# Kernel tuning notes

Measured on AMD Instinct MI355X. Metric: run time of the kernel, lower is better.

## Reference

```python
import jax, jax.numpy as jnp
import numpy as np

N_NODES = 50000
N_EDGES = 400000
N_GRAPHS = 128
IN_CH = 768
COND = 768
HID = 128
HEADS = 4


def _gat_conv(x, src, dst, W, att_src, att_dst, bias):
    """PyG-style GATConv (concat=True, negative_slope=0.2). x:[N,Fin], W:[Fin,H*D]."""
    N = x.shape[0]
    H, D = att_src.shape
    h = (x @ W).reshape(N, H, D)                      # [N,H,D]
    a_src = jnp.sum(h * att_src, axis=-1)             # [N,H]
    a_dst = jnp.sum(h * att_dst, axis=-1)             # [N,H]
    alpha = jax.nn.leaky_relu(a_src[src] + a_dst[dst], 0.2)   # [E,H]
    m = jax.ops.segment_max(alpha, dst, num_segments=N)       # per-dst max (stable softmax)
    alpha = jnp.exp(alpha - m[dst])
    s = jax.ops.segment_sum(alpha, dst, num_segments=N)
    alpha = alpha / (s[dst] + 1e-16)                  # PyG softmax eps
    msg = h[src] * alpha[:, :, None]                  # [E,H,D]
    out = jax.ops.segment_sum(msg, dst, num_segments=N)       # [N,H,D]
    return out.reshape(N, H * D) + bias


def setup_inputs() -> dict:
    key = jax.random.key(0)
    ks = jax.random.split(key, 12)

    def glorot(k, shape):
        fan = shape[0] + shape[-1]
        return jax.random.normal(k, shape, jnp.float32) * jnp.sqrt(2.0 / fan)

    x = jax.random.normal(ks[0], (N_NODES, IN_CH), jnp.float32)
    substring_embed = jax.random.normal(ks[1], (N_GRAPHS, COND), jnp.float32)
    edge_index = jax.random.randint(ks[2], (2, N_EDGES), 0, N_NODES)
    batch = jnp.sort(jax.random.randint(ks[3], (N_NODES,), 0, N_GRAPHS))

    W1 = glorot(ks[4], (IN_CH + COND, HEADS * HID))
    att_src1 = glorot(ks[5], (HEADS, HID))
    att_dst1 = glorot(ks[6], (HEADS, HID))
    b1 = jnp.zeros((HEADS * HID,), jnp.float32)

    W2 = glorot(ks[7], (HEADS * HID, 1 * HID))
    att_src2 = glorot(ks[8], (1, HID))
    att_dst2 = glorot(ks[9], (1, HID))
    b2 = jnp.zeros((HID,), jnp.float32)

    out_W = glorot(ks[10], (HID, 1))
    out_b = jnp.zeros((1,), jnp.float32)

    return {"x": x, "substring_embed": substring_embed,
            "W1": W1, "att_src1": att_src1, "att_dst1": att_dst1, "b1": b1,
            "W2": W2, "att_src2": att_src2, "att_dst2": att_dst2, "b2": b2,
            "out_W": out_W, "out_b": out_b,
            "edge_index": edge_index, "batch": batch}


def reference(x, substring_embed, W1, att_src1, att_dst1, b1,
              W2, att_src2, att_dst2, b2, out_W, out_b,
              edge_index, batch):
    N = x.shape[0]
    loops = jnp.arange(N)                              # PyG add_self_loops=True
    src = jnp.concatenate([edge_index[0], loops])
    dst = jnp.concatenate([edge_index[1], loops])

    h = jnp.concatenate([x, substring_embed[batch]], axis=-1)   # [N, IN+COND]
    h = jax.nn.relu(_gat_conv(h, src, dst, W1, att_src1, att_dst1, b1))
    h = jax.nn.relu(_gat_conv(h, src, dst, W2, att_src2, att_dst2, b2))
    out = (h @ out_W + out_b)[:, 0]                    # squeeze(-1) -> [N]
    return out
```

## Files before the change

### kernel.cpp

```cpp
#include <hip/hip_runtime.h>
#include <hip/hip_bf16.h>
#include <cstdint>
#include <cstddef>

#define NN 50000
#define NE 400000
#define NG 128
#define INCH 768
#define CONDCH 768
#define HIDD 128
#define NHEAD 4
#define F1 (NHEAD * HIDD)
#define F2 HIDD
#define MPAD 50176
#define CAP 64

typedef unsigned short ushort_t;
typedef float f32x4 __attribute__((ext_vector_type(4)));
typedef __bf16 bf16x8 __attribute__((ext_vector_type(8)));

typedef const void __attribute__((address_space(1))) as1_void;
typedef void __attribute__((address_space(3))) as3_void;

__device__ __forceinline__ void gload_lds16(const void* g, void* l) {
    __builtin_amdgcn_global_load_lds((as1_void*)g, (as3_void*)l, 16, 0, 0);
}

__device__ __forceinline__ ushort_t f2bf(float f) {
    uint32_t u = __float_as_uint(f);
    uint32_t r = (u + 0x7fffu + ((u >> 16) & 1u)) >> 16;
    return (ushort_t)r;
}
__device__ __forceinline__ uint32_t pack2(float a, float b) {
    return (uint32_t)f2bf(a) | ((uint32_t)f2bf(b) << 16);
}
__device__ __forceinline__ float bf_lo(uint32_t u) { return __uint_as_float(u << 16); }
__device__ __forceinline__ float bf_hi(uint32_t u) { return __uint_as_float(u & 0xffff0000u); }

#define R1 (F1 * INCH)
#define R2 (R1 + F1 * CONDCH)
#define R3 (R2 + F2 * F1)
#define CND4 (NG * CONDCH / 4)
__global__ __launch_bounds__(256) void k_prep(
    const float* __restrict__ W1, const float* __restrict__ W2, const float* __restrict__ cond,
    ushort_t* __restrict__ W1aT, ushort_t* __restrict__ W1cT, ushort_t* __restrict__ W2T,
    ushort_t* __restrict__ condb, int* __restrict__ cursor, int* __restrict__ csr_src)
{
    int idx = blockIdx.x * blockDim.x + threadIdx.x;
    if (idx < NN) {
        cursor[idx] = 1;
        csr_src[(size_t)idx * CAP] = idx;
    }
    if (idx < CND4) {
        float4 v = *(const float4*)(cond + (size_t)idx * 4);
        ushort4 o;
        o.x = f2bf(v.x); o.y = f2bf(v.y); o.z = f2bf(v.z); o.w = f2bf(v.w);
        *(ushort4*)(condb + (size_t)idx * 4) = o;
    }
    if (idx >= R3) return;
    if (idx < R1) {
        int n = idx / INCH, k = idx % INCH;
        W1aT[idx] = f2bf(W1[(size_t)k * F1 + n]);
    } else if (idx < R2) {
        int j = idx - R1;
        int n = j / CONDCH, k = j % CONDCH;
        W1cT[j] = f2bf(W1[(size_t)(INCH + k) * F1 + n]);
    } else {
        int j = idx - R2;
        int n = j / F1, k = j % F1;
        W2T[j] = f2bf(W2[(size_t)k * F2 + n]);
    }
}

__global__ __launch_bounds__(256) void k_scat(const int* __restrict__ ei,
                                              int* __restrict__ cursor,
                                              int* __restrict__ csr_src) {
    int e = blockIdx.x * blockDim.x + threadIdx.x;
    if (e >= NE) return;
    int src = ei[e];
    int dst = ei[NE + e];
    int pos = atomicAdd(&cursor[dst], 1);
    csr_src[(size_t)dst * CAP + pos] = src;
}

__global__ __launch_bounds__(256) void k_cvt8(const float* __restrict__ in,
                                              ushort_t* __restrict__ out, long n8) {
    long i = (long)blockIdx.x * blockDim.x + threadIdx.x;
    if (i >= n8) return;
    float4 v0 = *(const float4*)(in + i * 8);
    float4 v1 = *(const float4*)(in + i * 8 + 4);
    uint4 o;
    o.x = pack2(v0.x, v0.y);
    o.y = pack2(v0.z, v0.w);
    o.z = pack2(v1.x, v1.y);
    o.w = pack2(v1.z, v1.w);
    *(uint4*)(out + i * 8) = o;
}

template <int TM, bool ADD_GATHER, bool OUT_BF16, bool FUSE_ATT>
__global__ __launch_bounds__(TM * 2) void k_mgemm(
    const ushort_t* __restrict__ A, const ushort_t* __restrict__ BT, void* __restrict__ Cv,
    int M, int N, int K, int nBN,
    const float* __restrict__ G, const int* __restrict__ gidx,
    const float* __restrict__ attS, const float* __restrict__ attD,
    float* __restrict__ aS, float* __restrict__ aD, int attStride)
{
    constexpr int SA = TM * 64;
    constexpr int SB = 8192;
    __shared__ __align__(16) char smem[2 * SA + 2 * SB];
    char* sA = smem;
    char* sB = smem + 2 * SA;

    const int nwg = gridDim.x;
    const int orig = blockIdx.x;
    const int q = nwg >> 3, r = nwg & 7;
    const int xcd = orig & 7, sid = orig >> 3;
    const int wg = (xcd < r ? xcd * (q + 1) : r * (q + 1) + (xcd - r) * q) + sid;
    const int bx = wg / nBN, by = wg % nBN;

    const int tid = threadIdx.x;
    const int lane = tid & 63;
    const int wave = tid >> 6;
    const int wr = wave >> 1, wc = wave & 1;
    const int m0 = bx * TM, n0 = by * 128;

    const int sr = tid >> 2;
    const int sc = (tid & 3) * 8;
    const ushort_t* gA = A + (size_t)(m0 + sr) * K + sc;
    const ushort_t* gB = BT + (size_t)(n0 + sr) * K + sc;
    const int ldsw = wave * 1024;

    const int a_off = (wr * 64 + (lane & 15)) * 64 + (lane >> 4) * 16;
    const int b_off = (wc * 64 + (lane & 15)) * 64 + (lane >> 4) * 16;

    auto STAGE = [&](int kt, int b) {
        char* dA = sA + b * SA + ldsw;
        gload_lds16(gA + kt, dA);
        gload_lds16(gA + (size_t)(TM / 2) * K + kt, dA + SA / 2);
        char* dB = sB + b * SB + ldsw;
        gload_lds16(gB + kt, dB);
        if (TM == 128)
            gload_lds16(gB + (size_t)64 * K + kt, dB + 4096);
    };

    f32x4 acc[4][4];
#pragma unroll
    for (int i = 0; i < 4; i++)
#pragma unroll
        for (int j = 0; j < 4; j++) acc[i][j] = 0.f;

    STAGE(0, 0);
    const int nt = K / 32;
    for (int t = 0; t < nt; t++) {
        const int cur = t & 1;
        asm volatile("s_waitcnt vmcnt(0)" ::: "memory");
        __builtin_amdgcn_s_barrier();
        __builtin_amdgcn_sched_barrier(0);
        if (t + 1 < nt) STAGE((t + 1) * 32, cur ^ 1);
        bf16x8 af[4], bfr[4];
#pragma unroll
        for (int i = 0; i < 4; i++) af[i]  = *(const bf16x8*)(sA + cur * SA + a_off + i * 1024);
#pragma unroll
        for (int j = 0; j < 4; j++) bfr[j] = *(const bf16x8*)(sB + cur * SB + b_off + j * 1024);
#pragma unroll
        for (int i = 0; i < 4; i++)
#pragma unroll
            for (int j = 0; j < 4; j++)
                acc[i][j] = __builtin_amdgcn_mfma_f32_16x16x32_bf16(af[i], bfr[j], acc[i][j], 0, 0, 0);
    }

    float asv[4], adv[4];
    if (FUSE_ATT) {
#pragma unroll
        for (int j = 0; j < 4; j++) {
            int col = wc * 64 + j * 16 + (lane & 15);
            asv[j] = attS[by * 128 + col];
            adv[j] = attD[by * 128 + col];
        }
    }
    float* redS = (float*)smem;
    float* redD = (float*)smem + 2 * TM;

#pragma unroll
    for (int i = 0; i < 4; i++) {
        int mbase = m0 + wr * 64 + i * 16 + (lane >> 4) * 4;
#pragma unroll
        for (int rr = 0; rr < 4; rr++) {
            int m = mbase + rr;
            if (m >= M) continue;
            const float* grow = nullptr;
            if (ADD_GATHER) grow = G + (size_t)gidx[m] * N;
            float vs = 0.f, vd = 0.f;
#pragma unroll
            for (int j = 0; j < 4; j++) {
                int n = n0 + wc * 64 + j * 16 + (lane & 15);
                float v = acc[i][j][rr];
                if (ADD_GATHER) v += grow[n];
                if (OUT_BF16) ((ushort_t*)Cv)[(size_t)m * N + n] = f2bf(v);
                else          ((float*)Cv)[(size_t)m * N + n] = v;
                if (FUSE_ATT) { vs = fmaf(v, asv[j], vs); vd = fmaf(v, adv[j], vd); }
            }
            if (FUSE_ATT) {
#pragma unroll
                for (int o = 1; o < 16; o <<= 1) { vs += __shfl_xor(vs, o); vd += __shfl_xor(vd, o); }
                if ((lane & 15) == 0) {
                    int mloc = wr * 64 + i * 16 + (lane >> 4) * 4 + rr;
                    redS[wc * TM + mloc] = vs;
                    redD[wc * TM + mloc] = vd;
                }
            }
        }
    }
    if (FUSE_ATT) {
        __syncthreads();
        int sd = tid >= TM ? 1 : 0, mloc = tid & (TM - 1);
        int m = m0 + mloc;
        if (m < M) {
            const float* rb = sd ? redD : redS;
            float v = rb[mloc] + rb[TM + mloc];
            (sd ? aD : aS)[(size_t)m * attStride + by] = v;
        }
    }
}

__global__ __launch_bounds__(256) void k_agg1(
    const ushort_t* __restrict__ h1, const float* __restrict__ a_src, const float* __restrict__ a_dst,
    const int* __restrict__ cnt, const int* __restrict__ csr_src,
    const float* __restrict__ b1, ushort_t* __restrict__ g1)
{
    const int n = blockIdx.x * 4 + (threadIdx.x >> 6);
    const int lane = threadIdx.x & 63;
    const int head = lane >> 4;
    const int beg = n * CAP;
    const int end = beg + cnt[n];
    const float4 ad = *(const float4*)(a_dst + (size_t)n * 4);

    float mx[4] = {-1e30f, -1e30f, -1e30f, -1e30f};
    for (int p = beg + lane; p < end; p += 64) {
        int src = csr_src[p];
        float4 as = *(const float4*)(a_src + (size_t)src * 4);
        float v;
        v = as.x + ad.x; v = v >= 0.f ? v : 0.2f * v; mx[0] = fmaxf(mx[0], v);
        v = as.y + ad.y; v = v >= 0.f ? v : 0.2f * v; mx[1] = fmaxf(mx[1], v);
        v = as.z + ad.z; v = v >= 0.f ? v : 0.2f * v; mx[2] = fmaxf(mx[2], v);
        v = as.w + ad.w; v = v >= 0.f ? v : 0.2f * v; mx[3] = fmaxf(mx[3], v);
    }
#pragma unroll
    for (int o = 32; o; o >>= 1) {
        mx[0] = fmaxf(mx[0], __shfl_xor(mx[0], o));
        mx[1] = fmaxf(mx[1], __shfl_xor(mx[1], o));
        mx[2] = fmaxf(mx[2], __shfl_xor(mx[2], o));
        mx[3] = fmaxf(mx[3], __shfl_xor(mx[3], o));
    }
    const float m   = (head & 1) ? ((head & 2) ? mx[3] : mx[1]) : ((head & 2) ? mx[2] : mx[0]);
    const float adh = (head & 1) ? ((head & 2) ? ad.w : ad.y)   : ((head & 2) ? ad.z : ad.x);

    float ssum = 0.f;
    float a[8] = {0.f, 0.f, 0.f, 0.f, 0.f, 0.f, 0.f, 0.f};
    int p = beg;
#define LREL(l) ((l) >= 0.f ? (l) : 0.2f * (l))
#define ACC8(c, u) \
        a[0] = fmaf(c, bf_lo(u.x), a[0]); a[1] = fmaf(c, bf_hi(u.x), a[1]); \
        a[2] = fmaf(c, bf_lo(u.y), a[2]); a[3] = fmaf(c, bf_hi(u.y), a[3]); \
        a[4] = fmaf(c, bf_lo(u.z), a[4]); a[5] = fmaf(c, bf_hi(u.z), a[5]); \
        a[6] = fmaf(c, bf_lo(u.w), a[6]); a[7] = fmaf(c, bf_hi(u.w), a[7]);
    for (; p + 3 < end; p += 4) {
        int4 s4 = *(const int4*)(csr_src + p);
        uint4 u0 = *(const uint4*)(h1 + (size_t)s4.x * F1 + lane * 8);
        uint4 u1 = *(const uint4*)(h1 + (size_t)s4.y * F1 + lane * 8);
        uint4 u2 = *(const uint4*)(h1 + (size_t)s4.z * F1 + lane * 8);
        uint4 u3 = *(const uint4*)(h1 + (size_t)s4.w * F1 + lane * 8);
        float c0 = expf(LREL(a_src[s4.x * 4 + head] + adh) - m);
        float c1 = expf(LREL(a_src[s4.y * 4 + head] + adh) - m);
        float c2 = expf(LREL(a_src[s4.z * 4 + head] + adh) - m);
        float c3 = expf(LREL(a_src[s4.w * 4 + head] + adh) - m);
        ssum += c0 + c1 + c2 + c3;
        ACC8(c0, u0) ACC8(c1, u1) ACC8(c2, u2) ACC8(c3, u3)
    }
    for (; p < end; p++) {
        int s0 = csr_src[p];
        uint4 u0 = *(const uint4*)(h1 + (size_t)s0 * F1 + lane * 8);
        float c0 = expf(LREL(a_src[s0 * 4 + head] + adh) - m);
        ssum += c0;
        ACC8(c0, u0)
    }
#undef ACC8
    const float inv = 1.0f / (ssum + 1e-16f);
    const int ch = lane * 8;
    float4 bA = *(const float4*)(b1 + ch);
    float4 bB = *(const float4*)(b1 + ch + 4);
    uint4 ov;
    ov.x = pack2(fmaxf(fmaf(a[0], inv, bA.x), 0.f), fmaxf(fmaf(a[1], inv, bA.y), 0.f));
    ov.y = pack2(fmaxf(fmaf(a[2], inv, bA.z), 0.f), fmaxf(fmaf(a[3], inv, bA.w), 0.f));
    ov.z = pack2(fmaxf(fmaf(a[4], inv, bB.x), 0.f), fmaxf(fmaf(a[5], inv, bB.y), 0.f));
    ov.w = pack2(fmaxf(fmaf(a[6], inv, bB.z), 0.f), fmaxf(fmaf(a[7], inv, bB.w), 0.f));
    *(uint4*)(g1 + (size_t)n * F1 + ch) = ov;
}

__global__ __launch_bounds__(256) void k_agg2(
    const ushort_t* __restrict__ h2, const float* __restrict__ a_src, const float* __restrict__ a_dst,
    const int* __restrict__ cnt, const int* __restrict__ csr_src,
    const float* __restrict__ b2, const float* __restrict__ outW, const float* __restrict__ outb,
    float* __restrict__ out)
{
    const int n = blockIdx.x * 4 + (threadIdx.x >> 6);
    const int lane = threadIdx.x & 63;
    const int beg = n * CAP;
    const int end = beg + cnt[n];
    const float ad = a_dst[n];

    float mx = -1e30f;
    for (int p = beg + lane; p < end; p += 64) {
        float v = a_src[csr_src[p]] + ad;
        v = v >= 0.f ? v : 0.2f * v;
        mx = fmaxf(mx, v);
    }
#pragma unroll
    for (int o = 32; o; o >>= 1) mx = fmaxf(mx, __shfl_xor(mx, o));

    float ssum = 0.f;
    float a0 = 0.f, a1 = 0.f;
    int p = beg;
    for (; p + 3 < end; p += 4) {
        int4 s4 = *(const int4*)(csr_src + p);
        uint32_t u0 = *(const uint32_t*)(h2 + (size_t)s4.x * F2 + lane * 2);
        uint32_t u1 = *(const uint32_t*)(h2 + (size_t)s4.y * F2 + lane * 2);
        uint32_t u2 = *(const uint32_t*)(h2 + (size_t)s4.z * F2 + lane * 2);
        uint32_t u3 = *(const uint32_t*)(h2 + (size_t)s4.w * F2 + lane * 2);
        float c0 = expf(LREL(a_src[s4.x] + ad) - mx);
        float c1 = expf(LREL(a_src[s4.y] + ad) - mx);
        float c2 = expf(LREL(a_src[s4.z] + ad) - mx);
        float c3 = expf(LREL(a_src[s4.w] + ad) - mx);
        ssum += c0 + c1 + c2 + c3;
        a0 = fmaf(c0, bf_lo(u0), a0); a1 = fmaf(c0, bf_hi(u0), a1);
        a0 = fmaf(c1, bf_lo(u1), a0); a1 = fmaf(c1, bf_hi(u1), a1);
        a0 = fmaf(c2, bf_lo(u2), a0); a1 = fmaf(c2, bf_hi(u2), a1);
        a0 = fmaf(c3, bf_lo(u3), a0); a1 = fmaf(c3, bf_hi(u3), a1);
    }
    for (; p < end; p++) {
        int s0 = csr_src[p];
        uint32_t u0 = *(const uint32_t*)(h2 + (size_t)s0 * F2 + lane * 2);
        float c0 = expf(LREL(a_src[s0] + ad) - mx);
        ssum += c0;
        a0 = fmaf(c0, bf_lo(u0), a0); a1 = fmaf(c0, bf_hi(u0), a1);
    }
    const float inv = 1.0f / (ssum + 1e-16f);
    float v0 = fmaf(a0, inv, b2[lane * 2]);     v0 = v0 > 0.f ? v0 : 0.f;
    float v1 = fmaf(a1, inv, b2[lane * 2 + 1]); v1 = v1 > 0.f ? v1 : 0.f;
    float pr = v0 * outW[lane * 2] + v1 * outW[lane * 2 + 1];
    for (int o = 32; o; o >>= 1) pr += __shfl_xor(pr, o);
    if (lane == 0) out[n] = pr + outb[0];
}

extern "C" void kernel_launch(void* const* d_in, const int* in_sizes, int n_in,
                              void* d_out, int out_size, void* d_ws, size_t ws_size,
                              hipStream_t stream)
{
    const float* x        = (const float*)d_in[0];
    const float* cond     = (const float*)d_in[1];
    const float* W1       = (const float*)d_in[2];
    const float* att_src1 = (const float*)d_in[3];
    const float* att_dst1 = (const float*)d_in[4];
    const float* b1       = (const float*)d_in[5];
    const float* W2       = (const float*)d_in[6];
    const float* att_src2 = (const float*)d_in[7];
    const float* att_dst2 = (const float*)d_in[8];
    const float* b2       = (const float*)d_in[9];
    const float* outW     = (const float*)d_in[10];
    const float* outb     = (const float*)d_in[11];
    const int*   ei       = (const int*)d_in[12];
    const int*   batch    = (const int*)d_in[13];
    float* out = (float*)d_out;

    char* ws = (char*)d_ws;
    size_t off = 0;
    auto alloc = [&](size_t bytes) { void* p = ws + off; off += (bytes + 255) & ~size_t(255); return p; };
    ushort_t* xb      = (ushort_t*)alloc((size_t)MPAD * INCH * 2);
    ushort_t* condb   = (ushort_t*)alloc((size_t)NG * CONDCH * 2);
    ushort_t* W1aT    = (ushort_t*)alloc((size_t)F1 * INCH * 2);
    ushort_t* W1cT    = (ushort_t*)alloc((size_t)F1 * CONDCH * 2);
    ushort_t* W2T     = (ushort_t*)alloc((size_t)F2 * F1 * 2);
    float*    C2      = (float*)alloc((size_t)NG * F1 * 4);
    ushort_t* h1b     = (ushort_t*)alloc((size_t)NN * F1 * 2);
    float*    a_src1  = (float*)alloc((size_t)NN * NHEAD * 4);
    float*    a_dst1  = (float*)alloc((size_t)NN * NHEAD * 4);
    int*      cursor  = (int*)alloc((size_t)NN * 4);
    int*      csr_src = (int*)alloc((size_t)NN * CAP * 4);
    ushort_t* h2b     = (ushort_t*)alloc((size_t)NN * F2 * 2);
    float*    a_src2  = (float*)alloc((size_t)NN * 4);
    float*    a_dst2  = (float*)alloc((size_t)NN * 4);
    ushort_t* g1b     = xb;
    (void)ws_size;

    k_prep<<<(R3 + 255) / 256, 256, 0, stream>>>(W1, W2, cond, W1aT, W1cT, W2T, condb,
                                                 cursor, csr_src);

    k_scat<<<(NE + 255) / 256, 256, 0, stream>>>(ei, cursor, csr_src);

    {
        long n8 = (long)NN * INCH / 8;
        k_cvt8<<<(int)((n8 + 255) / 256), 256, 0, stream>>>(x, xb, n8);
    }

    k_mgemm<128, false, false, false><<<4, 256, 0, stream>>>(
        condb, W1cT, C2, NG, F1, CONDCH, 4,
        nullptr, nullptr, nullptr, nullptr, nullptr, nullptr, 0);
    k_mgemm<256, true, true, true><<<(MPAD / 256) * 4, 512, 0, stream>>>(
        xb, W1aT, h1b, NN, F1, INCH, 4,
        C2, batch, att_src1, att_dst1, a_src1, a_dst1, NHEAD);
    k_agg1<<<NN / 4, 256, 0, stream>>>(h1b, a_src1, a_dst1, cursor, csr_src, b1, g1b);
    k_mgemm<128, false, true, true><<<MPAD / 128, 256, 0, stream>>>(
        g1b, W2T, h2b, NN, F2, F1, 1,
        nullptr, nullptr, att_src2, att_dst2, a_src2, a_dst2, 1);
    k_agg2<<<NN / 4, 256, 0, stream>>>(h2b, a_src2, a_dst2, cursor, csr_src, b2, outW, outb, out);
}
```

Measured before the change: 277.5 us.

## Fuse fp32-to-bf16 conversion of x into the layer-1 GEMM A-tile load

Removes the separate k_cvt8 pass and its bf16 staging buffer for x. The first GEMM now streams fp32 rows of x straight into LDS with an XOR-swizzled layout, clamping padded rows to the last valid row. It converts to bf16 while building the MFMA fragments. This avoids a full read plus write of the converted input, but doubles A-tile LDS usage and global A traffic per tile. It also adds conversion work inside the inner loop and a min-blocks hint to launch bounds.

```diff
diff --git a/kernel.cpp b/kernel.cpp
--- a/kernel.cpp
+++ b/kernel.cpp
@@ -83,33 +83,21 @@
     csr_src[(size_t)dst * CAP + pos] = src;
 }
 
-__global__ __launch_bounds__(256) void k_cvt8(const float* __restrict__ in,
-                                              ushort_t* __restrict__ out, long n8) {
-    long i = (long)blockIdx.x * blockDim.x + threadIdx.x;
-    if (i >= n8) return;
-    float4 v0 = *(const float4*)(in + i * 8);
-    float4 v1 = *(const float4*)(in + i * 8 + 4);
-    uint4 o;
-    o.x = pack2(v0.x, v0.y);
-    o.y = pack2(v0.z, v0.w);
-    o.z = pack2(v1.x, v1.y);
-    o.w = pack2(v1.z, v1.w);
-    *(uint4*)(out + i * 8) = o;
-}
-
-template <int TM, bool ADD_GATHER, bool OUT_BF16, bool FUSE_ATT>
-__global__ __launch_bounds__(TM * 2) void k_mgemm(
-    const ushort_t* __restrict__ A, const ushort_t* __restrict__ BT, void* __restrict__ Cv,
+template <int TM, bool A_F32, bool ADD_GATHER, bool OUT_BF16, bool FUSE_ATT>
+__global__ __launch_bounds__(TM * 2, 4) void k_mgemm(
+    const ushort_t* __restrict__ A, const float* __restrict__ Af, int Arowmax,
+    const ushort_t* __restrict__ BT, void* __restrict__ Cv,
     int M, int N, int K, int nBN,
     const float* __restrict__ G, const int* __restrict__ gidx,
     const float* __restrict__ attS, const float* __restrict__ attD,
     float* __restrict__ aS, float* __restrict__ aD, int attStride)
 {
-    constexpr int SA = TM * 64;
+    constexpr int SAB = A_F32 ? TM * 128 : TM * 64;
     constexpr int SB = 8192;
-    __shared__ __align__(16) char smem[2 * SA + 2 * SB];
+    constexpr int ISS_BYTES = TM * 32;
+    __shared__ __align__(16) char smem[2 * SAB + 2 * SB];
     char* sA = smem;
-    char* sB = smem + 2 * SA;
+    char* sB = smem + 2 * SAB;
 
     const int nwg = gridDim.x;
     const int orig = blockIdx.x;
@@ -126,17 +114,35 @@
 
     const int sr = tid >> 2;
     const int sc = (tid & 3) * 8;
-    const ushort_t* gA = A + (size_t)(m0 + sr) * K + sc;
+    const ushort_t* gA = A_F32 ? nullptr : (A + (size_t)(m0 + sr) * K + sc);
     const ushort_t* gB = BT + (size_t)(n0 + sr) * K + sc;
     const int ldsw = wave * 1024;
 
+    const float* gAf_base[4];
+    if constexpr (A_F32) {
+        const int rowInIss = tid >> 3;
+        const int chunkS = (tid & 7) ^ (rowInIss & 7);
+#pragma unroll
+        for (int j = 0; j < 4; j++) {
+            int rr = m0 + j * (TM / 4) + rowInIss;
+            if (rr > Arowmax) rr = Arowmax;
+            gAf_base[j] = Af + (size_t)rr * K + chunkS * 4;
+        }
+    }
+
     const int a_off = (wr * 64 + (lane & 15)) * 64 + (lane >> 4) * 16;
     const int b_off = (wc * 64 + (lane & 15)) * 64 + (lane >> 4) * 16;
 
     auto STAGE = [&](int kt, int b) {
-        char* dA = sA + b * SA + ldsw;
-        gload_lds16(gA + kt, dA);
-        gload_lds16(gA + (size_t)(TM / 2) * K + kt, dA + SA / 2);
+        if constexpr (A_F32) {
+#pragma unroll
+            for (int j = 0; j < 4; j++)
+                gload_lds16(gAf_base[j] + kt, sA + b * SAB + j * ISS_BYTES + ldsw);
+        } else {
+            char* dA = sA + b * SAB + ldsw;
+            gload_lds16(gA + kt, dA);
+            gload_lds16(gA + (size_t)(TM / 2) * K + kt, dA + SAB / 2);
+        }
         char* dB = sB + b * SB + ldsw;
         gload_lds16(gB + kt, dB);
         if (TM == 128)
@@ -158,8 +164,24 @@
         __builtin_amdgcn_sched_barrier(0);
         if (t + 1 < nt) STAGE((t + 1) * 32, cur ^ 1);
         bf16x8 af[4], bfr[4];
-#pragma unroll
-        for (int i = 0; i < 4; i++) af[i]  = *(const bf16x8*)(sA + cur * SA + a_off + i * 1024);
+        if constexpr (A_F32) {
+            const int q32 = (lane >> 4) * 32;
+#pragma unroll
+            for (int i = 0; i < 4; i++) {
+                int rw = wr * 64 + i * 16 + (lane & 15);
+                int sw = (rw & 7) << 4;
+                const char* base = sA + cur * SAB + rw * 128;
+                float4 lo = *(const float4*)(base + (q32 ^ sw));
+                float4 hi = *(const float4*)(base + ((q32 + 16) ^ sw));
+                bf16x8 v;
+                v[0] = (__bf16)lo.x; v[1] = (__bf16)lo.y; v[2] = (__bf16)lo.z; v[3] = (__bf16)lo.w;
+                v[4] = (__bf16)hi.x; v[5] = (__bf16)hi.y; v[6] = (__bf16)hi.z; v[7] = (__bf16)hi.w;
+                af[i] = v;
+            }
+        } else {
+#pragma unroll
+            for (int i = 0; i < 4; i++) af[i] = *(const bf16x8*)(sA + cur * SAB + a_off + i * 1024);
+        }
 #pragma unroll
         for (int j = 0; j < 4; j++) bfr[j] = *(const bf16x8*)(sB + cur * SB + b_off + j * 1024);
 #pragma unroll
@@ -375,7 +397,6 @@
     char* ws = (char*)d_ws;
     size_t off = 0;
     auto alloc = [&](size_t bytes) { void* p = ws + off; off += (bytes + 255) & ~size_t(255); return p; };
-    ushort_t* xb      = (ushort_t*)alloc((size_t)MPAD * INCH * 2);
     ushort_t* condb   = (ushort_t*)alloc((size_t)NG * CONDCH * 2);
     ushort_t* W1aT    = (ushort_t*)alloc((size_t)F1 * INCH * 2);
     ushort_t* W1cT    = (ushort_t*)alloc((size_t)F1 * CONDCH * 2);
@@ -386,10 +407,10 @@
     float*    a_dst1  = (float*)alloc((size_t)NN * NHEAD * 4);
     int*      cursor  = (int*)alloc((size_t)NN * 4);
     int*      csr_src = (int*)alloc((size_t)NN * CAP * 4);
+    ushort_t* g1b     = (ushort_t*)alloc((size_t)MPAD * F1 * 2);
     ushort_t* h2b     = (ushort_t*)alloc((size_t)NN * F2 * 2);
     float*    a_src2  = (float*)alloc((size_t)NN * 4);
     float*    a_dst2  = (float*)alloc((size_t)NN * 4);
-    ushort_t* g1b     = xb;
     (void)ws_size;
 
     k_prep<<<(R3 + 255) / 256, 256, 0, stream>>>(W1, W2, cond, W1aT, W1cT, W2T, condb,
@@ -397,20 +418,15 @@
 
     k_scat<<<(NE + 255) / 256, 256, 0, stream>>>(ei, cursor, csr_src);
 
-    {
-        long n8 = (long)NN * INCH / 8;
-        k_cvt8<<<(int)((n8 + 255) / 256), 256, 0, stream>>>(x, xb, n8);
-    }
-
-    k_mgemm<128, false, false, false><<<4, 256, 0, stream>>>(
-        condb, W1cT, C2, NG, F1, CONDCH, 4,
+    k_mgemm<128, false, false, false, false><<<4, 256, 0, stream>>>(
+        condb, nullptr, 0, W1cT, C2, NG, F1, CONDCH, 4,
         nullptr, nullptr, nullptr, nullptr, nullptr, nullptr, 0);
-    k_mgemm<256, true, true, true><<<(MPAD / 256) * 4, 512, 0, stream>>>(
-        xb, W1aT, h1b, NN, F1, INCH, 4,
+    k_mgemm<256, true, true, true, true><<<(MPAD / 256) * 4, 512, 0, stream>>>(
+        nullptr, x, NN - 1, W1aT, h1b, NN, F1, INCH, 4,
         C2, batch, att_src1, att_dst1, a_src1, a_dst1, NHEAD);
     k_agg1<<<NN / 4, 256, 0, stream>>>(h1b, a_src1, a_dst1, cursor, csr_src, b1, g1b);
-    k_mgemm<128, false, true, true><<<MPAD / 128, 256, 0, stream>>>(
-        g1b, W2T, h2b, NN, F2, F1, 1,
+    k_mgemm<128, false, false, true, true><<<MPAD / 128, 256, 0, stream>>>(
+        g1b, nullptr, 0, W2T, h2b, NN, F2, F1, 1,
         nullptr, nullptr, att_src2, att_dst2, a_src2, a_dst2, 1);
     k_agg2<<<NN / 4, 256, 0, stream>>>(h2b, a_src2, a_dst2, cursor, csr_src, b2, outW, outb, out);
 }
```

Measured after the change: 277.4 us, median of 2. No clear change (-0.1%).
